# Optimization experiments

Hardware: AMD Instinct MI355X
Metric: run time of the kernel (lower is better)

The kernel has to match this reference:

```python
import jax, jax.numpy as jnp
import numpy as np

EMBED_DIM = 1024
HEADS = 16
HEAD_DIM = EMBED_DIM // HEADS


def setup_inputs() -> dict:
    key = jax.random.key(0)
    k1, k2, k3, k4 = jax.random.split(key, 4)
    x = jax.random.normal(k1, (4, 2048, EMBED_DIM), dtype=jnp.float32)
    # nn.Linear weights stored as (out, in); apply as x @ W.T
    W_qkv = jax.random.normal(k2, (3 * EMBED_DIM, EMBED_DIM), dtype=jnp.float32) / np.sqrt(EMBED_DIM)
    W_out = jax.random.normal(k3, (EMBED_DIM, EMBED_DIM), dtype=jnp.float32) / np.sqrt(EMBED_DIM)
    b_out = jax.random.normal(k4, (EMBED_DIM,), dtype=jnp.float32) * 0.02
    return {"x": x, "W_qkv": W_qkv, "W_out": W_out, "b_out": b_out}


def reference(x, W_qkv, W_out, b_out):
    B, N, _ = x.shape
    qkv = jnp.einsum('bnd,ed->bne', x, W_qkv)  # (B, N, 3*E)
    q, k, v = jnp.split(qkv, 3, axis=-1)
    # (B, H, N, Dh)
    q = q.reshape(B, N, HEADS, HEAD_DIM).transpose(0, 2, 1, 3)
    k = k.reshape(B, N, HEADS, HEAD_DIM).transpose(0, 2, 1, 3)
    v = v.reshape(B, N, HEADS, HEAD_DIM).transpose(0, 2, 1, 3)
    scale = 1.0 / np.sqrt(HEAD_DIM).astype(np.float32)
    scores = jnp.einsum('bhqd,bhkd->bhqk', q, k) * scale  # (B, H, N, N)
    attn = jax.nn.softmax(scores, axis=-1)
    out = jnp.einsum('bhqk,bhkd->bhqd', attn, v)  # (B, H, N, Dh)
    out = out.transpose(0, 2, 1, 3).reshape(B, N, EMBED_DIM)
    return jnp.einsum('bne,oe->bno', out, W_out) + b_out
```

## Files before the change

### kernel.cpp

```cpp
#include <hip/hip_runtime.h>
#include <hip/hip_bf16.h>
#include <stdint.h>


typedef _Float16 half8 __attribute__((ext_vector_type(8)));
typedef _Float16 half4 __attribute__((ext_vector_type(4)));
typedef __fp16 fp16x2 __attribute__((ext_vector_type(2)));
typedef float floatx4 __attribute__((ext_vector_type(4)));

#define E 1024
#define NH 16
#define DH 64
#define SEQ 2048
#define BATCH 4

__device__ __forceinline__ void gload_lds16(const void* g, void* lds) {
  typedef __attribute__((address_space(1))) void gv;
  typedef __attribute__((address_space(3))) void lv;
  __builtin_amdgcn_global_load_lds((gv*)g, (lv*)lds, 16, 0, 0);
}

__device__ __forceinline__ float fast_exp2(float x) {
#if __has_builtin(__builtin_amdgcn_exp2f)
  return __builtin_amdgcn_exp2f(x);
#else
  return exp2f(x);
#endif
}

__device__ __forceinline__ float max3f(float a, float b, float c) {
  return fmaxf(fmaxf(a, b), c);
}

__global__ __launch_bounds__(256)
void cvt3_f32_f16(const float* __restrict__ a, _Float16* __restrict__ oa, int na,
                  const float* __restrict__ b, _Float16* __restrict__ ob, int nb,
                  const float* __restrict__ c, _Float16* __restrict__ oc, int nc) {
  int i = blockIdx.x * 256 + threadIdx.x;
  const float* in;
  _Float16* out;
  int idx;
  if (i < na) { in = a; out = oa; idx = i; }
  else if (i < na + nb) { in = b; out = ob; idx = i - na; }
  else if (i < na + nb + nc) { in = c; out = oc; idx = i - na - nb; }
  else return;
  const float4* p = (const float4*)in;
  float4 u = p[2 * idx], v = p[2 * idx + 1];
  half8 h;
  h[0] = (_Float16)u.x; h[1] = (_Float16)u.y; h[2] = (_Float16)u.z; h[3] = (_Float16)u.w;
  h[4] = (_Float16)v.x; h[5] = (_Float16)v.y; h[6] = (_Float16)v.z; h[7] = (_Float16)v.w;
  ((half8*)out)[idx] = h;
}

__global__ __launch_bounds__(256)
void gemm_qkv(const _Float16* __restrict__ A, const _Float16* __restrict__ W,
              _Float16* __restrict__ qo, _Float16* __restrict__ ko, _Float16* __restrict__ vt) {
  __shared__ __align__(16) _Float16 As[128 * 64];
  __shared__ __align__(16) _Float16 Bs[128 * 64];
  const int t = threadIdx.x;
  const int w = t >> 6, l = t & 63;
  const int wr = w >> 1, wc = w & 1;
  const int lr = l & 15, hi = l >> 4;
  const int tileRow = blockIdx.y * 128;
  const int tileCol = blockIdx.x * 128;
  const int ldsW = (t & ~63) * 16;
  floatx4 acc[4][4] = {};

  for (int k0 = 0; k0 < 1024; k0 += 64) {
    __syncthreads();
#pragma unroll
    for (int c = 0; c < 4; ++c) {
      int idx = c * 256 + t;
      int row = idx >> 3, g = idx & 7;
      gload_lds16(A + (size_t)(tileRow + row) * 1024 + k0 + g * 8, (char*)As + c * 4096 + ldsW);
      gload_lds16(W + (size_t)(tileCol + row) * 1024 + k0 + g * 8, (char*)Bs + c * 4096 + ldsW);
    }
    __syncthreads();
#pragma unroll
    for (int kk = 0; kk < 2; ++kk) {
      half8 af[4], bf[4];
#pragma unroll
      for (int m = 0; m < 4; ++m)
        af[m] = *(const half8*)(As + (wr * 64 + m * 16 + lr) * 64 + kk * 32 + hi * 8);
#pragma unroll
      for (int n = 0; n < 4; ++n)
        bf[n] = *(const half8*)(Bs + (wc * 64 + n * 16 + lr) * 64 + kk * 32 + hi * 8);
#pragma unroll
      for (int m = 0; m < 4; ++m)
#pragma unroll
        for (int n = 0; n < 4; ++n)
          acc[m][n] = __builtin_amdgcn_mfma_f32_16x16x32_f16(af[m], bf[n], acc[m][n], 0, 0, 0);
    }
  }
  const int sec = tileCol >> 10;
  const int b = tileRow >> 11;
  const int tokBase = (tileRow & 2047) + wr * 64;
  if (sec == 2) {
#pragma unroll
    for (int n = 0; n < 4; ++n) {
      int col = (tileCol & 1023) + wc * 64 + n * 16 + lr;
      int h = col >> 6, d = col & 63;
      _Float16* base = vt + (((size_t)b * NH + h) * DH + d) * SEQ + tokBase;
#pragma unroll
      for (int m = 0; m < 4; ++m) {
        half4 v;
#pragma unroll
        for (int j = 0; j < 4; ++j) v[j] = (_Float16)acc[m][n][j];
        *(half4*)(base + m * 16 + hi * 4) = v;
      }
    }
  } else {
    _Float16* dst = sec == 0 ? qo : ko;
    const float scaleq = sec == 0 ? 0.18033688011112042f : 1.0f;
#pragma unroll
    for (int n = 0; n < 4; ++n) {
      int col = (tileCol & 1023) + wc * 64 + n * 16 + lr;
      int h = col >> 6, d = col & 63;
      _Float16* base = dst + (((size_t)b * NH + h) * SEQ + tokBase) * DH + d;
#pragma unroll
      for (int m = 0; m < 4; ++m)
#pragma unroll
        for (int j = 0; j < 4; ++j)
          base[(size_t)(m * 16 + hi * 4 + j) * DH] = (_Float16)(acc[m][n][j] * scaleq);
    }
  }
}

__global__ __launch_bounds__(256, 3)
void attn(const _Float16* __restrict__ Q, const _Float16* __restrict__ Kg,
          const _Float16* __restrict__ VT, _Float16* __restrict__ O) {
  __shared__ __align__(16) _Float16 Ks[64 * 64];
  __shared__ __align__(16) _Float16 Vs[64 * 64];
  __shared__ __align__(16) _Float16 Ps[4][16 * 64];
  const int orig = blockIdx.x;
  const int nid = (orig & 7) * 128 + (orig >> 3);
  const int qt = nid & 15, bh = nid >> 4;
  const int t = threadIdx.x, w = t >> 6, l = t & 63;
  const int lr = l & 15, hi = l >> 4;
  const int ldsW = (t & ~63) * 16;
  const _Float16* qb = Q + ((size_t)bh * SEQ + qt * 128 + w * 32) * DH;
  half8 qf[2][2];
#pragma unroll
  for (int g = 0; g < 2; ++g) {
    qf[g][0] = *(const half8*)(qb + (g * 16 + lr) * DH + hi * 8);
    qf[g][1] = *(const half8*)(qb + (g * 16 + lr) * DH + 32 + hi * 8);
  }
  floatx4 o0[4] = {}, o1[4] = {};
  float m0 = 0.f, m1 = 0.f, l0 = 0.f, l1 = 0.f;
  const _Float16* kb = Kg + (size_t)bh * SEQ * DH;
  const _Float16* vb = VT + (size_t)bh * DH * SEQ;
  char* pw = (char*)&Ps[w][0];
  const int lrm = lr & 7;
  uint32_t wra[4], rda[2];
#pragma unroll
  for (int n = 0; n < 4; ++n)
    wra[n] = lr * 128 + ((((2 * n + (hi >> 1)) ^ lrm)) << 4) + (hi & 1) * 8;
#pragma unroll
  for (int kk = 0; kk < 2; ++kk)
    rda[kk] = lr * 128 + (((4 * kk + hi) ^ lrm) << 4);

  auto sm = [&](floatx4(&s)[4], float& mr, float& lsum, floatx4(&oa)[4], fp16x2(&pk)[4][2]) {
    float ma = max3f(s[0][0], s[0][1], s[0][2]);
    float mb = max3f(s[0][3], s[1][0], s[1][1]);
    float mc = max3f(s[1][2], s[1][3], s[2][0]);
    float md = max3f(s[2][1], s[2][2], s[2][3]);
    float me = max3f(s[3][0], s[3][1], s[3][2]);
    float mx = max3f(max3f(ma, mb, mc), fmaxf(md, me), s[3][3]);
    mx = fmaxf(mx, __shfl_xor(mx, 16));
    mx = fmaxf(mx, __shfl_xor(mx, 32));
    float rs = 0.f;
    if (__builtin_expect(__any(mx > 10.f), 0)) {
      float dm = fmaxf(mx, 0.f);
      float fac = fast_exp2(-dm);
      mr += dm;
      lsum *= fac;
#pragma unroll
      for (int j = 0; j < 4; ++j) {
        float fj = __shfl(fac, hi * 4 + j);
#pragma unroll
        for (int n = 0; n < 4; ++n) oa[n][j] *= fj;
      }
#pragma unroll
      for (int n = 0; n < 4; ++n) {
        float p0 = fast_exp2(s[n][0] - dm), p1 = fast_exp2(s[n][1] - dm);
        float p2 = fast_exp2(s[n][2] - dm), p3 = fast_exp2(s[n][3] - dm);
        pk[n][0] = __builtin_amdgcn_cvt_pkrtz(p0, p1);
        pk[n][1] = __builtin_amdgcn_cvt_pkrtz(p2, p3);
        rs += p0 + p1 + p2 + p3;
      }
    } else {
#pragma unroll
      for (int n = 0; n < 4; ++n) {
        float p0 = fast_exp2(s[n][0]), p1 = fast_exp2(s[n][1]);
        float p2 = fast_exp2(s[n][2]), p3 = fast_exp2(s[n][3]);
        pk[n][0] = __builtin_amdgcn_cvt_pkrtz(p0, p1);
        pk[n][1] = __builtin_amdgcn_cvt_pkrtz(p2, p3);
        rs += p0 + p1 + p2 + p3;
      }
    }
    lsum += rs;
  };

  auto proute = [&](fp16x2(&pk)[4][2], half8(&pf)[2]) {
#pragma unroll
    for (int n = 0; n < 4; ++n) {
      uint2 v;
      v.x = __builtin_bit_cast(uint32_t, pk[n][0]);
      v.y = __builtin_bit_cast(uint32_t, pk[n][1]);
      *(uint2*)(pw + wra[n]) = v;
    }
    pf[0] = *(const half8*)(pw + rda[0]);
    pf[1] = *(const half8*)(pw + rda[1]);
  };

  for (int kt = 0; kt < SEQ / 64; ++kt) {
    __syncthreads();
#pragma unroll
    for (int c = 0; c < 2; ++c) {
      int idx = c * 256 + t;
      int row = idx >> 3, g = idx & 7, gs = g ^ (row & 7);
      gload_lds16(kb + (size_t)(kt * 64 + row) * DH + gs * 8, (char*)Ks + c * 4096 + ldsW);
      gload_lds16(vb + (size_t)row * SEQ + kt * 64 + gs * 8, (char*)Vs + c * 4096 + ldsW);
    }
    __syncthreads();
    half8 af[8];
#pragma unroll
    for (int kk = 0; kk < 2; ++kk) {
      int gl = kk * 4 + hi;
#pragma unroll
      for (int n = 0; n < 4; ++n) {
        int key = n * 16 + lr;
        af[kk * 4 + n] = *(const half8*)((char*)Ks + key * 128 + ((gl ^ (key & 7)) << 4));
      }
    }
    floatx4 cb0 = {-m0, -m0, -m0, -m0};
    floatx4 s0[4] = {cb0, cb0, cb0, cb0};
    __builtin_amdgcn_s_setprio(1);
#pragma unroll
    for (int kk = 0; kk < 2; ++kk)
#pragma unroll
      for (int n = 0; n < 4; ++n)
        s0[n] = __builtin_amdgcn_mfma_f32_16x16x32_f16(af[kk * 4 + n], qf[0][kk], s0[n], 0, 0, 0);
    __builtin_amdgcn_s_setprio(0);
    fp16x2 pk[4][2];
    half8 pf[2];
    sm(s0, m0, l0, o0, pk);
    proute(pk, pf);
    floatx4 cb1 = {-m1, -m1, -m1, -m1};
    floatx4 s1[4] = {cb1, cb1, cb1, cb1};
    __builtin_amdgcn_s_setprio(1);
#pragma unroll
    for (int kk = 0; kk < 2; ++kk)
#pragma unroll
      for (int n = 0; n < 4; ++n)
        s1[n] = __builtin_amdgcn_mfma_f32_16x16x32_f16(af[kk * 4 + n], qf[1][kk], s1[n], 0, 0, 0);
    __builtin_amdgcn_s_setprio(0);
    half8 vf[8];
#pragma unroll
    for (int kk = 0; kk < 2; ++kk) {
      int gl = kk * 4 + hi;
#pragma unroll
      for (int n = 0; n < 4; ++n) {
        int d = n * 16 + lr;
        vf[kk * 4 + n] = *(const half8*)((char*)Vs + d * 128 + ((gl ^ (d & 7)) << 4));
      }
    }
    __builtin_amdgcn_s_setprio(1);
#pragma unroll
    for (int kk = 0; kk < 2; ++kk)
#pragma unroll
      for (int n = 0; n < 4; ++n)
        o0[n] = __builtin_amdgcn_mfma_f32_16x16x32_f16(pf[kk], vf[kk * 4 + n], o0[n], 0, 0, 0);
    __builtin_amdgcn_s_setprio(0);
    sm(s1, m1, l1, o1, pk);
    proute(pk, pf);
    __builtin_amdgcn_s_setprio(1);
#pragma unroll
    for (int kk = 0; kk < 2; ++kk)
#pragma unroll
      for (int n = 0; n < 4; ++n)
        o1[n] = __builtin_amdgcn_mfma_f32_16x16x32_f16(pf[kk], vf[kk * 4 + n], o1[n], 0, 0, 0);
    __builtin_amdgcn_s_setprio(0);
  }
  l0 += __shfl_xor(l0, 16); l0 += __shfl_xor(l0, 32);
  l1 += __shfl_xor(l1, 16); l1 += __shfl_xor(l1, 32);
  const int b = bh >> 4, h = bh & 15;
#pragma unroll
  for (int g = 0; g < 2; ++g) {
    const floatx4* oa = g == 0 ? o0 : o1;
    float lg = g == 0 ? l0 : l1;
#pragma unroll
    for (int j = 0; j < 4; ++j) {
      float lj = __shfl(lg, hi * 4 + j);
      float inv = 1.f / lj;
      int tok = qt * 128 + w * 32 + g * 16 + hi * 4 + j;
      _Float16* ob = O + ((size_t)b * SEQ + tok) * E + h * DH;
#pragma unroll
      for (int n = 0; n < 4; ++n) ob[n * 16 + lr] = (_Float16)(oa[n][j] * inv);
    }
  }
}

__global__ __launch_bounds__(256)
void gemm_out(const _Float16* __restrict__ A, const _Float16* __restrict__ W,
              const float* __restrict__ bias, float* __restrict__ out) {
  __shared__ __align__(16) _Float16 As[128 * 64];
  __shared__ __align__(16) _Float16 Bs[128 * 64];
  const int t = threadIdx.x;
  const int w = t >> 6, l = t & 63;
  const int wr = w >> 1, wc = w & 1;
  const int lr = l & 15, hi = l >> 4;
  const int tileRow = blockIdx.y * 128;
  const int tileCol = blockIdx.x * 128;
  const int ldsW = (t & ~63) * 16;
  floatx4 acc[4][4] = {};

  for (int k0 = 0; k0 < 1024; k0 += 64) {
    __syncthreads();
#pragma unroll
    for (int c = 0; c < 4; ++c) {
      int idx = c * 256 + t;
      int row = idx >> 3, g = idx & 7;
      gload_lds16(A + (size_t)(tileRow + row) * 1024 + k0 + g * 8, (char*)As + c * 4096 + ldsW);
      gload_lds16(W + (size_t)(tileCol + row) * 1024 + k0 + g * 8, (char*)Bs + c * 4096 + ldsW);
    }
    __syncthreads();
#pragma unroll
    for (int kk = 0; kk < 2; ++kk) {
      half8 af[4], bf[4];
#pragma unroll
      for (int m = 0; m < 4; ++m)
        af[m] = *(const half8*)(As + (wr * 64 + m * 16 + lr) * 64 + kk * 32 + hi * 8);
#pragma unroll
      for (int n = 0; n < 4; ++n)
        bf[n] = *(const half8*)(Bs + (wc * 64 + n * 16 + lr) * 64 + kk * 32 + hi * 8);
#pragma unroll
      for (int m = 0; m < 4; ++m)
#pragma unroll
        for (int n = 0; n < 4; ++n)
          acc[m][n] = __builtin_amdgcn_mfma_f32_16x16x32_f16(af[m], bf[n], acc[m][n], 0, 0, 0);
    }
  }
#pragma unroll
  for (int n = 0; n < 4; ++n) {
    int col = tileCol + wc * 64 + n * 16 + lr;
    float bv = bias[col];
#pragma unroll
    for (int m = 0; m < 4; ++m) {
      int row = tileRow + wr * 64 + m * 16 + hi * 4;
#pragma unroll
      for (int j = 0; j < 4; ++j)
        out[(size_t)(row + j) * E + col] = acc[m][n][j] + bv;
    }
  }
}

extern "C" void kernel_launch(void* const* d_in, const int* in_sizes, int n_in,
                              void* d_out, int out_size, void* d_ws, size_t ws_size,
                              hipStream_t stream) {
  const float* x = (const float*)d_in[0];
  const float* Wqkv = (const float*)d_in[1];
  const float* Wout = (const float*)d_in[2];
  const float* bout = (const float*)d_in[3];
  float* out = (float*)d_out;
  char* ws = (char*)d_ws;
  _Float16* x16 = (_Float16*)(ws);
  _Float16* q16 = (_Float16*)(ws + (16u << 20));
  _Float16* k16 = (_Float16*)(ws + (32u << 20));
  _Float16* vt16 = (_Float16*)(ws + (48u << 20));
  _Float16* wq16 = (_Float16*)(ws + (64u << 20));
  _Float16* wo16 = (_Float16*)(ws + (70u << 20));
  _Float16* ao16 = x16;

  int n8x = in_sizes[0] / 8, n8q = in_sizes[1] / 8, n8o = in_sizes[2] / 8;
  int n8 = n8x + n8q + n8o;
  cvt3_f32_f16<<<(n8 + 255) / 256, 256, 0, stream>>>(x, x16, n8x, Wqkv, wq16, n8q, Wout, wo16, n8o);
  gemm_qkv<<<dim3(24, 64), 256, 0, stream>>>(x16, wq16, q16, k16, vt16);
  attn<<<dim3(1024), 256, 0, stream>>>(q16, k16, vt16, ao16);
  gemm_out<<<dim3(8, 64), 256, 0, stream>>>(ao16, wo16, bout, out);
}
```

Baseline: 225.4 us.

## Restructure attention inner loop by kk halves and raise occupancy to 4 blocks

The K and V fragment loads move into per-kk halves (4 half8 registers instead of 8), and both query groups' score MFMAs are interleaved in each half. Softmax for both groups is now computed back to back before the PV MFMAs. Launch bounds are raised from 3 to 4 blocks per CU. The goal is lower register pressure and higher occupancy so latency hides better. The cost is a longer serial softmax section without MFMA work overlapping it, and possible spills under the tighter register cap.

```diff
diff --git a/kernel.cpp b/kernel.cpp
--- a/kernel.cpp
+++ b/kernel.cpp
@@ -126,7 +126,7 @@
   }
 }
 
-__global__ __launch_bounds__(256, 3)
+__global__ __launch_bounds__(256, 4)
 void attn(const _Float16* __restrict__ Q, const _Float16* __restrict__ Kg,
           const _Float16* __restrict__ VT, _Float16* __restrict__ O) {
   __shared__ __align__(16) _Float16 Ks[64 * 64];
@@ -223,64 +223,52 @@
       gload_lds16(vb + (size_t)row * SEQ + kt * 64 + gs * 8, (char*)Vs + c * 4096 + ldsW);
     }
     __syncthreads();
-    half8 af[8];
+    floatx4 cb0 = {-m0, -m0, -m0, -m0};
+    floatx4 cb1 = {-m1, -m1, -m1, -m1};
+    floatx4 s0[4] = {cb0, cb0, cb0, cb0};
+    floatx4 s1[4] = {cb1, cb1, cb1, cb1};
 #pragma unroll
     for (int kk = 0; kk < 2; ++kk) {
       int gl = kk * 4 + hi;
+      half8 afk[4];
 #pragma unroll
       for (int n = 0; n < 4; ++n) {
         int key = n * 16 + lr;
-        af[kk * 4 + n] = *(const half8*)((char*)Ks + key * 128 + ((gl ^ (key & 7)) << 4));
-      }
-    }
-    floatx4 cb0 = {-m0, -m0, -m0, -m0};
-    floatx4 s0[4] = {cb0, cb0, cb0, cb0};
-    __builtin_amdgcn_s_setprio(1);
-#pragma unroll
-    for (int kk = 0; kk < 2; ++kk)
-#pragma unroll
-      for (int n = 0; n < 4; ++n)
-        s0[n] = __builtin_amdgcn_mfma_f32_16x16x32_f16(af[kk * 4 + n], qf[0][kk], s0[n], 0, 0, 0);
-    __builtin_amdgcn_s_setprio(0);
+        afk[n] = *(const half8*)((char*)Ks + key * 128 + ((gl ^ (key & 7)) << 4));
+      }
+      __builtin_amdgcn_s_setprio(1);
+#pragma unroll
+      for (int n = 0; n < 4; ++n)
+        s0[n] = __builtin_amdgcn_mfma_f32_16x16x32_f16(afk[n], qf[0][kk], s0[n], 0, 0, 0);
+#pragma unroll
+      for (int n = 0; n < 4; ++n)
+        s1[n] = __builtin_amdgcn_mfma_f32_16x16x32_f16(afk[n], qf[1][kk], s1[n], 0, 0, 0);
+      __builtin_amdgcn_s_setprio(0);
+    }
     fp16x2 pk[4][2];
-    half8 pf[2];
+    half8 pf0[2], pf1[2];
     sm(s0, m0, l0, o0, pk);
-    proute(pk, pf);
-    floatx4 cb1 = {-m1, -m1, -m1, -m1};
-    floatx4 s1[4] = {cb1, cb1, cb1, cb1};
-    __builtin_amdgcn_s_setprio(1);
-#pragma unroll
-    for (int kk = 0; kk < 2; ++kk)
-#pragma unroll
-      for (int n = 0; n < 4; ++n)
-        s1[n] = __builtin_amdgcn_mfma_f32_16x16x32_f16(af[kk * 4 + n], qf[1][kk], s1[n], 0, 0, 0);
-    __builtin_amdgcn_s_setprio(0);
-    half8 vf[8];
+    proute(pk, pf0);
+    sm(s1, m1, l1, o1, pk);
+    proute(pk, pf1);
 #pragma unroll
     for (int kk = 0; kk < 2; ++kk) {
       int gl = kk * 4 + hi;
+      half8 vfk[4];
 #pragma unroll
       for (int n = 0; n < 4; ++n) {
         int d = n * 16 + lr;
-        vf[kk * 4 + n] = *(const half8*)((char*)Vs + d * 128 + ((gl ^ (d & 7)) << 4));
-      }
-    }
-    __builtin_amdgcn_s_setprio(1);
-#pragma unroll
-    for (int kk = 0; kk < 2; ++kk)
-#pragma unroll
-      for (int n = 0; n < 4; ++n)
-        o0[n] = __builtin_amdgcn_mfma_f32_16x16x32_f16(pf[kk], vf[kk * 4 + n], o0[n], 0, 0, 0);
-    __builtin_amdgcn_s_setprio(0);
-    sm(s1, m1, l1, o1, pk);
-    proute(pk, pf);
-    __builtin_amdgcn_s_setprio(1);
-#pragma unroll
-    for (int kk = 0; kk < 2; ++kk)
-#pragma unroll
-      for (int n = 0; n < 4; ++n)
-        o1[n] = __builtin_amdgcn_mfma_f32_16x16x32_f16(pf[kk], vf[kk * 4 + n], o1[n], 0, 0, 0);
-    __builtin_amdgcn_s_setprio(0);
+        vfk[n] = *(const half8*)((char*)Vs + d * 128 + ((gl ^ (d & 7)) << 4));
+      }
+      __builtin_amdgcn_s_setprio(1);
+#pragma unroll
+      for (int n = 0; n < 4; ++n)
+        o0[n] = __builtin_amdgcn_mfma_f32_16x16x32_f16(pf0[kk], vfk[n], o0[n], 0, 0, 0);
+#pragma unroll
+      for (int n = 0; n < 4; ++n)
+        o1[n] = __builtin_amdgcn_mfma_f32_16x16x32_f16(pf1[kk], vfk[n], o1[n], 0, 0, 0);
+      __builtin_amdgcn_s_setprio(0);
+    }
   }
   l0 += __shfl_xor(l0, 16); l0 += __shfl_xor(l0, 32);
   l1 += __shfl_xor(l1, 16); l1 += __shfl_xor(l1, 32);
```

New measurement: 237.0 us. 5.1% more time.
